# Kernel tuning notes

Measured on AMD Instinct MI355X. Metric: run time of the kernel, lower is better.

The kernel has to match this reference:

```python
import jax, jax.numpy as jnp
import numpy as np

D, NH, NL, NP, NLAYERS = 256, 8, 4, 4, 6
DH = D // NH
SHAPES = [(76, 100), (38, 50), (19, 25), (10, 13)]
STARTS = [int(s) for s in np.cumsum([0] + [h * w for h, w in SHAPES])[:-1]]
LQ = sum(h * w for h, w in SHAPES)
B = 2


def _layernorm(x, g, b, eps=1e-5):
    m = x.mean(-1, keepdims=True)
    v = ((x - m) ** 2).mean(-1, keepdims=True)
    return (x - m) * jax.lax.rsqrt(v + eps) * g + b


def _ref_points():
    pts = []
    for H, W in SHAPES:
        ry = (jnp.arange(H, dtype=jnp.float32) + 0.5) / H
        rx = (jnp.arange(W, dtype=jnp.float32) + 0.5) / W
        gy, gx = jnp.meshgrid(ry, rx, indexing='ij')
        pts.append(jnp.stack([gx.ravel(), gy.ravel()], -1))
    ref = jnp.concatenate(pts, 0)  # [LQ, 2] (x, y)
    return jnp.broadcast_to(ref[:, None, :], (LQ, NL, 2))


def _bilinear(v, loc, H, W):
    # v: [BN, H*W, DH]; loc: [BN, N, 2] normalized (x, y).
    # Matches torch grid_sample(align_corners=False, padding='zeros') with grid=2*loc-1.
    px = loc[..., 0] * W - 0.5
    py = loc[..., 1] * H - 0.5
    x0f = jnp.floor(px)
    y0f = jnp.floor(py)
    lx = px - x0f
    ly = py - y0f
    x0 = x0f.astype(jnp.int32)
    y0 = y0f.astype(jnp.int32)
    out = jnp.zeros(loc.shape[:-1] + (DH,), v.dtype)
    for dy, dx, w in ((0, 0, (1 - ly) * (1 - lx)), (0, 1, (1 - ly) * lx), (1, 0, ly * (1 - lx)), (1, 1, ly * lx)):
        xi = x0 + dx
        yi = y0 + dy
        valid = (xi >= 0) & (xi < W) & (yi >= 0) & (yi < H)
        idx = jnp.clip(yi, 0, H - 1) * W + jnp.clip(xi, 0, W - 1)
        g = jnp.take_along_axis(v, idx[..., None], axis=1)  # [BN, N, DH]
        out = out + g * (w * valid)[..., None]
    return out


def _layer(src, pos, ref, p):
    q = src + pos
    value = (src @ p['w_val'] + p['b_val']).reshape(B, LQ, NH, DH)
    off = (q @ p['w_off'] + p['b_off']).reshape(B, LQ, NH, NL, NP, 2)
    aw = jax.nn.softmax((q @ p['w_attn'] + p['b_attn']).reshape(B, LQ, NH, NL * NP), -1)
    aw = aw.reshape(B, LQ, NH, NL, NP)
    norm = jnp.array([[w, h] for h, w in SHAPES], jnp.float32)  # [NL, 2] = (W, H)
    loc = ref[None, :, None, :, None, :] + off / norm[None, None, None, :, None, :]  # [B,LQ,NH,NL,NP,2]
    v_t = value.transpose(0, 2, 1, 3).reshape(B * NH, LQ, DH)
    out = jnp.zeros((B, NH, LQ, DH), src.dtype)
    for l, (H, W) in enumerate(SHAPES):
        vl = v_t[:, STARTS[l]:STARTS[l] + H * W]
        locl = loc[:, :, :, l].transpose(0, 2, 1, 3, 4).reshape(B * NH, LQ * NP, 2)
        g = _bilinear(vl, locl, H, W).reshape(B, NH, LQ, NP, DH)
        out = out + jnp.einsum('bhqp,bhqpd->bhqd', aw[:, :, :, l].transpose(0, 2, 1, 3), g)
    attn = out.transpose(0, 2, 1, 3).reshape(B, LQ, D) @ p['w_out'] + p['b_out']
    src = _layernorm(src + attn, p['ln1_g'], p['ln1_b'])
    ffn = jax.nn.relu(src @ p['w_ffn1'] + p['b_ffn1']) @ p['w_ffn2'] + p['b_ffn2']
    return _layernorm(src + ffn, p['ln2_g'], p['ln2_b'])


def setup_inputs() -> dict:
    key = jax.random.key(0)
    ks = jax.random.split(key, 16)
    inp = {}
    for i, (H, W) in enumerate(SHAPES):
        inp[f'src{i}'] = jax.random.normal(ks[i], (B, D, H, W), jnp.float32)
        inp[f'pos{i}'] = jax.random.normal(ks[4 + i], (B, D, H, W), jnp.float32)
    inp['level_embed'] = jax.random.normal(ks[8], (NL, D), jnp.float32)
    s = 0.02
    inp['w_off'] = jax.random.normal(ks[9], (NLAYERS, D, NH * NL * NP * 2), jnp.float32) * s
    inp['b_off'] = jnp.zeros((NLAYERS, NH * NL * NP * 2), jnp.float32)
    inp['w_attn'] = jax.random.normal(ks[10], (NLAYERS, D, NH * NL * NP), jnp.float32) * s
    inp['b_attn'] = jnp.zeros((NLAYERS, NH * NL * NP), jnp.float32)
    inp['w_val'] = jax.random.normal(ks[11], (NLAYERS, D, D), jnp.float32) * s
    inp['b_val'] = jnp.zeros((NLAYERS, D), jnp.float32)
    inp['w_out'] = jax.random.normal(ks[12], (NLAYERS, D, D), jnp.float32) * s
    inp['b_out'] = jnp.zeros((NLAYERS, D), jnp.float32)
    inp['ln1_g'] = jnp.ones((NLAYERS, D), jnp.float32)
    inp['ln1_b'] = jnp.zeros((NLAYERS, D), jnp.float32)
    inp['w_ffn1'] = jax.random.normal(ks[13], (NLAYERS, D, 1024), jnp.float32) * s
    inp['b_ffn1'] = jnp.zeros((NLAYERS, 1024), jnp.float32)
    inp['w_ffn2'] = jax.random.normal(ks[14], (NLAYERS, 1024, D), jnp.float32) * s
    inp['b_ffn2'] = jnp.zeros((NLAYERS, D), jnp.float32)
    inp['ln2_g'] = jnp.ones((NLAYERS, D), jnp.float32)
    inp['ln2_b'] = jnp.zeros((NLAYERS, D), jnp.float32)
    return inp


def reference(src0, src1, src2, src3, pos0, pos1, pos2, pos3, level_embed,
              w_off, b_off, w_attn, b_attn, w_val, b_val, w_out, b_out,
              ln1_g, ln1_b, w_ffn1, b_ffn1, w_ffn2, b_ffn2, ln2_g, ln2_b):
    srcs = [src0, src1, src2, src3]
    poss = [pos0, pos1, pos2, pos3]
    src_flat = jnp.concatenate(
        [s.reshape(B, D, -1).transpose(0, 2, 1) + level_embed[l][None, None] for l, s in enumerate(srcs)], 1)
    pos_flat = jnp.concatenate([p.reshape(B, D, -1).transpose(0, 2, 1) for p in poss], 1)
    ref = _ref_points()
    x = src_flat
    for i in range(NLAYERS):
        p = dict(w_off=w_off[i], b_off=b_off[i], w_attn=w_attn[i], b_attn=b_attn[i],
                 w_val=w_val[i], b_val=b_val[i], w_out=w_out[i], b_out=b_out[i],
                 ln1_g=ln1_g[i], ln1_b=ln1_b[i], w_ffn1=w_ffn1[i], b_ffn1=b_ffn1[i],
                 w_ffn2=w_ffn2[i], b_ffn2=b_ffn2[i], ln2_g=ln2_g[i], ln2_b=ln2_b[i])
        x = _layer(x, pos_flat, ref, p)
    return x  # [B, LQ, D] encoded memory
```

## Files before the change

### kernel.cpp

```cpp
#include <hip/hip_runtime.h>
#include <math.h>

#define LQ 10105
#define BATCH 2
#define NLAYERS 6
#define NTOK (BATCH * LQ)

typedef __attribute__((ext_vector_type(8))) short bf16x8;
typedef __attribute__((ext_vector_type(4))) float f32x4;

__device__ inline unsigned short f2bf_rne(float f) {
    unsigned u = __float_as_uint(f);
    unsigned r = u + 0x7fffu + ((u >> 16) & 1u);
    return (unsigned short)(r >> 16);
}
__device__ inline float bf2f(unsigned short h) {
    return __uint_as_float((unsigned)h << 16);
}

__global__ __launch_bounds__(256)
void flatten_k(const float* __restrict__ src, const float* __restrict__ pos,
               const float* __restrict__ lvl, float* __restrict__ src_flat,
               float* __restrict__ pos_flat, int HW, int start)
{
    int hw = blockIdx.x;
    int b  = blockIdx.y;
    int d  = threadIdx.x;
    float sv = src[((size_t)b * 256 + d) * HW + hw];
    float pv = pos[((size_t)b * 256 + d) * HW + hw];
    size_t o = ((size_t)(b * LQ + start + hw)) * 256 + d;
    src_flat[o] = sv + lvl[d];
    pos_flat[o] = pv;
}

__global__ __launch_bounds__(256)
void wsplit_k(const float* __restrict__ W, unsigned short* __restrict__ Th,
              unsigned short* __restrict__ Tl, int K, int N,
              long srcStride, long dstStride)
{
    __shared__ float t[32][33];
    int layer = blockIdx.z;
    int n0 = blockIdx.x * 32, k0 = blockIdx.y * 32;
    int tx = threadIdx.x & 31, ty = threadIdx.x >> 5;
    const float* Wsrc = W + (size_t)layer * srcStride;
    #pragma unroll
    for (int i = 0; i < 4; ++i)
        t[ty + i * 8][tx] = Wsrc[(size_t)(k0 + ty + i * 8) * N + n0 + tx];
    __syncthreads();
    unsigned short* th = Th + (size_t)layer * dstStride;
    unsigned short* tl = Tl + (size_t)layer * dstStride;
    #pragma unroll
    for (int i = 0; i < 4; ++i) {
        int n = n0 + ty + i * 8;
        float v = t[tx][ty + i * 8];
        unsigned short h = f2bf_rne(v);
        th[(size_t)n * K + k0 + tx] = h;
        tl[(size_t)n * K + k0 + tx] = f2bf_rne(v - bf2f(h));
    }
}

__global__ void boa_k(const float* __restrict__ b_off,
                      const float* __restrict__ b_attn, float* __restrict__ boa)
{
    int l = blockIdx.x, t = threadIdx.x;
    boa[l * 384 + t] = (t < 256) ? b_off[l * 256 + t] : b_attn[l * 128 + (t - 256)];
}

template<bool HAS_A2, bool RELU, bool HAS_RES>
__global__ __launch_bounds__(256)
void gemm_mfma(const float* __restrict__ A, const float* __restrict__ A2,
               const unsigned short* __restrict__ Bh,
               const unsigned short* __restrict__ Bl,
               const float* __restrict__ bias, const float* __restrict__ Res,
               float* __restrict__ C, int M, int N, int K)
{
    __shared__ unsigned short sAh[128 * 32];
    __shared__ unsigned short sAl[128 * 32];
    __shared__ unsigned short sBh[128 * 32];
    __shared__ unsigned short sBl[128 * 32];

    const int tid = threadIdx.x;
    const int m0 = blockIdx.x * 128;
    const int n0 = blockIdx.y * 128;

    const int w  = tid >> 6;
    const int l  = tid & 63;
    const int wm = (w >> 1) * 64;
    const int wn = (w & 1) * 64;
    const int lr = l & 15;
    const int kb = (l >> 4) * 8;
    const int rr = (l >> 4) * 4;

    const int sm = tid >> 1;
    const int sk = (tid & 1) * 16;
    const int arow = m0 + sm;
    const bool aok = arow < M;

    f32x4 acc[4][4];
    #pragma unroll
    for (int i = 0; i < 4; ++i)
        #pragma unroll
        for (int j = 0; j < 4; ++j)
            acc[i][j] = (f32x4){0.f, 0.f, 0.f, 0.f};

    for (int kt = 0; kt < K; kt += 32) {
        float va[16];
        if (aok) {
            const float* ap = &A[(size_t)arow * K + kt + sk];
            *(float4*)&va[0]  = *(const float4*)(ap + 0);
            *(float4*)&va[4]  = *(const float4*)(ap + 4);
            *(float4*)&va[8]  = *(const float4*)(ap + 8);
            *(float4*)&va[12] = *(const float4*)(ap + 12);
            if (HAS_A2) {
                const float* ap2 = &A2[(size_t)arow * K + kt + sk];
                float4 t0 = *(const float4*)(ap2 + 0);
                float4 t1 = *(const float4*)(ap2 + 4);
                float4 t2 = *(const float4*)(ap2 + 8);
                float4 t3 = *(const float4*)(ap2 + 12);
                va[0] += t0.x; va[1] += t0.y; va[2]  += t0.z; va[3]  += t0.w;
                va[4] += t1.x; va[5] += t1.y; va[6]  += t1.z; va[7]  += t1.w;
                va[8] += t2.x; va[9] += t2.y; va[10] += t2.z; va[11] += t2.w;
                va[12]+= t3.x; va[13]+= t3.y; va[14] += t3.z; va[15] += t3.w;
            }
        } else {
            #pragma unroll
            for (int j = 0; j < 16; ++j) va[j] = 0.f;
        }
        const unsigned short* bph = &Bh[(size_t)(n0 + sm) * K + kt + sk];
        const unsigned short* bpl = &Bl[(size_t)(n0 + sm) * K + kt + sk];
        bf16x8 vbh0 = *(const bf16x8*)(bph);
        bf16x8 vbh1 = *(const bf16x8*)(bph + 8);
        bf16x8 vbl0 = *(const bf16x8*)(bpl);
        bf16x8 vbl1 = *(const bf16x8*)(bpl + 8);

        bf16x8 ah0, ah1, al0, al1;
        #pragma unroll
        for (int j = 0; j < 8; ++j) {
            float v0 = va[j], v1 = va[8 + j];
            unsigned short h0 = (unsigned short)(__float_as_uint(v0) >> 16);
            unsigned short h1 = (unsigned short)(__float_as_uint(v1) >> 16);
            ah0[j] = (short)h0;
            ah1[j] = (short)h1;
            float r0 = v0 - bf2f(h0);
            float r1 = v1 - bf2f(h1);
            al0[j] = (short)(unsigned short)(__float_as_uint(r0) >> 16);
            al1[j] = (short)(unsigned short)(__float_as_uint(r1) >> 16);
        }

        __syncthreads();
        *(bf16x8*)&sAh[sm * 32 + sk]     = ah0;
        *(bf16x8*)&sAh[sm * 32 + sk + 8] = ah1;
        *(bf16x8*)&sAl[sm * 32 + sk]     = al0;
        *(bf16x8*)&sAl[sm * 32 + sk + 8] = al1;
        *(bf16x8*)&sBh[sm * 32 + sk]     = vbh0;
        *(bf16x8*)&sBh[sm * 32 + sk + 8] = vbh1;
        *(bf16x8*)&sBl[sm * 32 + sk]     = vbl0;
        *(bf16x8*)&sBl[sm * 32 + sk + 8] = vbl1;
        __syncthreads();

        bf16x8 fah[4], fal[4];
        #pragma unroll
        for (int mf = 0; mf < 4; ++mf) {
            int off = (wm + mf * 16 + lr) * 32 + kb;
            fah[mf] = *(const bf16x8*)&sAh[off];
            fal[mf] = *(const bf16x8*)&sAl[off];
        }
        #pragma unroll
        for (int nf = 0; nf < 4; ++nf) {
            int boff = (wn + nf * 16 + lr) * 32 + kb;
            bf16x8 fbh = *(const bf16x8*)&sBh[boff];
            bf16x8 fbl = *(const bf16x8*)&sBl[boff];
            #pragma unroll
            for (int mf = 0; mf < 4; ++mf) {
                f32x4 c = acc[mf][nf];
                c = __builtin_amdgcn_mfma_f32_16x16x32_bf16(fah[mf], fbh, c, 0, 0, 0);
                c = __builtin_amdgcn_mfma_f32_16x16x32_bf16(fah[mf], fbl, c, 0, 0, 0);
                c = __builtin_amdgcn_mfma_f32_16x16x32_bf16(fal[mf], fbh, c, 0, 0, 0);
                acc[mf][nf] = c;
            }
        }
    }

    #pragma unroll
    for (int nf = 0; nf < 4; ++nf) {
        int col = n0 + wn + nf * 16 + lr;
        float bs = bias[col];
        #pragma unroll
        for (int mf = 0; mf < 4; ++mf) {
            int rowb = m0 + wm + mf * 16 + rr;
            #pragma unroll
            for (int r = 0; r < 4; ++r) {
                int row = rowb + r;
                if (row < M) {
                    float v = acc[mf][nf][r] + bs;
                    if (HAS_RES) v += Res[(size_t)row * N + col];
                    if (RELU) v = fmaxf(v, 0.f);
                    C[(size_t)row * N + col] = v;
                }
            }
        }
    }
}

__global__ __launch_bounds__(256)
void sample_k(const float* __restrict__ val, const float* __restrict__ oab,
              float* __restrict__ out)
{
    const int Hs[4] = {76, 38, 19, 10};
    const int Ws[4] = {100, 50, 25, 13};
    const int ST[4] = {0, 7600, 9500, 9975};

    int bid = blockIdx.x;
    int xcd = bid & 7;
    const int qch = LQ >> 3;
    const int rem = LQ & 7;
    int q = (xcd < rem ? xcd * (qch + 1) : rem * (qch + 1) + (xcd - rem) * qch)
            + (bid >> 3);
    int b = blockIdx.y;
    int tid = threadIdx.x;

    __shared__ int2 s_iw[512];

    if (tid < 128) {
        int h = tid >> 4, pt = tid & 15, lvl = pt >> 2, p = pt & 3;
        int lq, local;
        if (q < 7600)      { lq = 0; local = q; }
        else if (q < 9500) { lq = 1; local = q - 7600; }
        else if (q < 9975) { lq = 2; local = q - 9500; }
        else               { lq = 3; local = q - 9975; }
        int Wq = Ws[lq], Hq = Hs[lq];
        int ry = local / Wq, rx = local - ry * Wq;
        float refx = (rx + 0.5f) / (float)Wq;
        float refy = (ry + 0.5f) / (float)Hq;

        size_t rowb = (size_t)(b * LQ + q) * 384;
        float logit = oab[rowb + 256 + h * 16 + pt];
        float mx = logit;
        mx = fmaxf(mx, __shfl_xor(mx, 1, 64));
        mx = fmaxf(mx, __shfl_xor(mx, 2, 64));
        mx = fmaxf(mx, __shfl_xor(mx, 4, 64));
        mx = fmaxf(mx, __shfl_xor(mx, 8, 64));
        float e = expf(logit - mx);
        float s = e;
        s += __shfl_xor(s, 1, 64);
        s += __shfl_xor(s, 2, 64);
        s += __shfl_xor(s, 4, 64);
        s += __shfl_xor(s, 8, 64);
        float aw = e / s;

        float ox = oab[rowb + h * 32 + lvl * 8 + p * 2];
        float oy = oab[rowb + h * 32 + lvl * 8 + p * 2 + 1];
        int W = Ws[lvl], H = Hs[lvl], st = ST[lvl];
        float px = refx * (float)W + ox - 0.5f;
        float py = refy * (float)H + oy - 0.5f;
        float x0f = floorf(px), y0f = floorf(py);
        float lx = px - x0f, ly = py - y0f;
        int x0 = (int)x0f, y0 = (int)y0f;
        int x1 = x0 + 1, y1 = y0 + 1;
        float ax0 = ((x0 >= 0) & (x0 < W)) ? (1.f - lx) : 0.f;
        float ax1 = ((x1 >= 0) & (x1 < W)) ? lx : 0.f;
        float ay0 = ((y0 >= 0) & (y0 < H)) ? (1.f - ly) : 0.f;
        float ay1 = ((y1 >= 0) & (y1 < H)) ? ly : 0.f;
        int cx0 = min(max(x0, 0), W - 1), cx1 = min(max(x1, 0), W - 1);
        int cy0 = min(max(y0, 0), H - 1), cy1 = min(max(y1, 0), H - 1);
        int i00 = st + cy0 * W + cx0, i01 = st + cy0 * W + cx1;
        int i10 = st + cy1 * W + cx0, i11 = st + cy1 * W + cx1;
        int base4 = tid * 4;
        s_iw[base4 + 0] = make_int2(i00, __float_as_int(aw * ay0 * ax0));
        s_iw[base4 + 1] = make_int2(i01, __float_as_int(aw * ay0 * ax1));
        s_iw[base4 + 2] = make_int2(i10, __float_as_int(aw * ay1 * ax0));
        s_iw[base4 + 3] = make_int2(i11, __float_as_int(aw * ay1 * ax1));
    }
    __syncthreads();

    int lane   = tid & 63;
    int wv     = tid >> 6;
    int h      = wv * 2 + (lane >> 5);
    int half   = lane & 31;
    int corner = half >> 3;
    int c4     = half & 7;
    const float* vb = val + (size_t)(b * LQ) * 256 + h * 32 + c4 * 4;
    int sbase = h * 64 + corner;

    float4 acc = make_float4(0.f, 0.f, 0.f, 0.f);
    #pragma unroll
    for (int pt = 0; pt < 16; ++pt) {
        int2 iw = s_iw[sbase + pt * 4];
        float wgt = __int_as_float(iw.y);
        float4 v = *(const float4*)&vb[(size_t)iw.x * 256];
        acc.x += wgt * v.x; acc.y += wgt * v.y;
        acc.z += wgt * v.z; acc.w += wgt * v.w;
    }
    acc.x += __shfl_xor(acc.x, 8, 64);  acc.y += __shfl_xor(acc.y, 8, 64);
    acc.z += __shfl_xor(acc.z, 8, 64);  acc.w += __shfl_xor(acc.w, 8, 64);
    acc.x += __shfl_xor(acc.x, 16, 64); acc.y += __shfl_xor(acc.y, 16, 64);
    acc.z += __shfl_xor(acc.z, 16, 64); acc.w += __shfl_xor(acc.w, 16, 64);

    if (corner == 0)
        *(float4*)&out[(size_t)(b * LQ + q) * 256 + h * 32 + c4 * 4] = acc;
}

__global__ __launch_bounds__(256)
void ln_k(const float* __restrict__ x, const float* __restrict__ g,
          const float* __restrict__ bt, float* __restrict__ out, int nrows)
{
    int row = blockIdx.x * 4 + (threadIdx.x >> 6);
    int lane = threadIdx.x & 63;
    if (row >= nrows) return;

    float4 v = *(const float4*)&x[(size_t)row * 256 + lane * 4];
    float s = v.x + v.y + v.z + v.w;
    #pragma unroll
    for (int o = 32; o > 0; o >>= 1) s += __shfl_down(s, o, 64);
    s = __shfl(s, 0, 64);
    float m = s * (1.0f / 256.0f);
    float cx = v.x - m, cy = v.y - m, cz = v.z - m, cw = v.w - m;
    float s2 = cx * cx + cy * cy + cz * cz + cw * cw;
    #pragma unroll
    for (int o = 32; o > 0; o >>= 1) s2 += __shfl_down(s2, o, 64);
    s2 = __shfl(s2, 0, 64);
    float rstd = rsqrtf(s2 * (1.0f / 256.0f) + 1e-5f);

    float4 gv = *(const float4*)&g[lane * 4];
    float4 bv = *(const float4*)&bt[lane * 4];
    float4 r;
    r.x = cx * rstd * gv.x + bv.x;
    r.y = cy * rstd * gv.y + bv.y;
    r.z = cz * rstd * gv.z + bv.z;
    r.w = cw * rstd * gv.w + bv.w;
    *(float4*)&out[(size_t)row * 256 + lane * 4] = r;
}

extern "C" void kernel_launch(void* const* d_in, const int* in_sizes, int n_in,
                              void* d_out, int out_size, void* d_ws, size_t ws_size,
                              hipStream_t stream)
{
    const float* src_in[4] = {(const float*)d_in[0], (const float*)d_in[2],
                              (const float*)d_in[4], (const float*)d_in[6]};
    const float* pos_in[4] = {(const float*)d_in[1], (const float*)d_in[3],
                              (const float*)d_in[5], (const float*)d_in[7]};
    const float* lvl    = (const float*)d_in[8];
    const float* w_off  = (const float*)d_in[9];
    const float* b_off  = (const float*)d_in[10];
    const float* w_attn = (const float*)d_in[11];
    const float* b_attn = (const float*)d_in[12];
    const float* w_val  = (const float*)d_in[13];
    const float* b_val  = (const float*)d_in[14];
    const float* w_out  = (const float*)d_in[15];
    const float* b_out  = (const float*)d_in[16];
    const float* ln1_g  = (const float*)d_in[17];
    const float* ln1_b  = (const float*)d_in[18];
    const float* w_ffn1 = (const float*)d_in[19];
    const float* b_ffn1 = (const float*)d_in[20];
    const float* w_ffn2 = (const float*)d_in[21];
    const float* b_ffn2 = (const float*)d_in[22];
    const float* ln2_g  = (const float*)d_in[23];
    const float* ln2_b  = (const float*)d_in[24];

    float* ws    = (float*)d_ws;
    float* src   = ws;
    float* pos   = src   + (size_t)NTOK * 256;
    float* preln = pos   + (size_t)NTOK * 256;
    float* uni   = preln + (size_t)NTOK * 256;
    float* valb  = uni;
    float* oab   = uni + (size_t)NTOK * 256;
    float* samp  = oab + (size_t)NTOK * 384;
    float* ffnb  = uni;
    float* boa   = uni + (size_t)NTOK * 1024;
    unsigned short* Wh = (unsigned short*)(boa + 6 * 384);
    const long WL = 753664;
    unsigned short* Wl = Wh + (size_t)NLAYERS * WL;
    const long O_VAL = 0, O_OFF = 65536, O_ATT = 131072, O_OUT = 163840,
               O_F1 = 229376, O_F2 = 491520;

    wsplit_k<<<dim3(8, 8, 6),  256, 0, stream>>>(w_val,  Wh + O_VAL, Wl + O_VAL, 256, 256,  65536, WL);
    wsplit_k<<<dim3(8, 8, 6),  256, 0, stream>>>(w_off,  Wh + O_OFF, Wl + O_OFF, 256, 256,  65536, WL);
    wsplit_k<<<dim3(4, 8, 6),  256, 0, stream>>>(w_attn, Wh + O_ATT, Wl + O_ATT, 256, 128,  32768, WL);
    wsplit_k<<<dim3(8, 8, 6),  256, 0, stream>>>(w_out,  Wh + O_OUT, Wl + O_OUT, 256, 256,  65536, WL);
    wsplit_k<<<dim3(32, 8, 6), 256, 0, stream>>>(w_ffn1, Wh + O_F1,  Wl + O_F1,  256, 1024, 262144, WL);
    wsplit_k<<<dim3(8, 32, 6), 256, 0, stream>>>(w_ffn2, Wh + O_F2,  Wl + O_F2,  1024, 256, 262144, WL);
    boa_k<<<dim3(6), dim3(384), 0, stream>>>(b_off, b_attn, boa);

    const int HWs[4] = {7600, 1900, 475, 130};
    const int STt[4] = {0, 7600, 9500, 9975};
    for (int l = 0; l < 4; ++l) {
        dim3 g(HWs[l], BATCH);
        flatten_k<<<g, 256, 0, stream>>>(src_in[l], pos_in[l], lvl + l * 256,
                                         src, pos, HWs[l], STt[l]);
    }

    const int MB = (NTOK + 127) / 128;
    const int LNB = (NTOK + 3) / 4;
    dim3 blk(256);

    for (int i = 0; i < NLAYERS; ++i) {
        const unsigned short* whL = Wh + (size_t)i * WL;
        const unsigned short* wlL = Wl + (size_t)i * WL;
        const float* bv  = b_val  + (size_t)i * 256;
        const float* bou = b_out  + (size_t)i * 256;
        const float* l1g = ln1_g  + (size_t)i * 256;
        const float* l1b = ln1_b  + (size_t)i * 256;
        const float* bf1 = b_ffn1 + (size_t)i * 1024;
        const float* bf2 = b_ffn2 + (size_t)i * 256;
        const float* l2g = ln2_g  + (size_t)i * 256;
        const float* l2b = ln2_b  + (size_t)i * 256;

        gemm_mfma<false, false, false><<<dim3(MB, 2), blk, 0, stream>>>(
            src, nullptr, whL + O_VAL, wlL + O_VAL, bv, nullptr, valb, NTOK, 256, 256);
        gemm_mfma<true, false, false><<<dim3(MB, 3), blk, 0, stream>>>(
            src, pos, whL + O_OFF, wlL + O_OFF, boa + (size_t)i * 384, nullptr,
            oab, NTOK, 384, 256);
        sample_k<<<dim3(LQ, BATCH), blk, 0, stream>>>(valb, oab, samp);
        gemm_mfma<false, false, true><<<dim3(MB, 2), blk, 0, stream>>>(
            samp, nullptr, whL + O_OUT, wlL + O_OUT, bou, src, preln, NTOK, 256, 256);
        ln_k<<<dim3(LNB), blk, 0, stream>>>(preln, l1g, l1b, src, NTOK);
        gemm_mfma<false, true, false><<<dim3(MB, 8), blk, 0, stream>>>(
            src, nullptr, whL + O_F1, wlL + O_F1, bf1, nullptr, ffnb, NTOK, 1024, 256);
        gemm_mfma<false, false, true><<<dim3(MB, 2), blk, 0, stream>>>(
            ffnb, nullptr, whL + O_F2, wlL + O_F2, bf2, src, preln, NTOK, 256, 1024);
        float* dst = (i == NLAYERS - 1) ? (float*)d_out : src;
        ln_k<<<dim3(LNB), blk, 0, stream>>>(preln, l2g, l2b, dst, NTOK);
    }
}
```

Baseline: 1.922 ms.

## Store value/sample/FFN intermediates in bf16, add XCD tile remap and LDS padding

The value projection, sampled features and FFN hidden activations are now written in bf16 instead of fp32. The consuming GEMMs read bf16 A directly, dropping the A low-part plane and one of three MFMAs per fragment. The GEMM also moves to a 1D grid with an XCD-aware block-to-tile remap, and pads LDS rows to 40 to reduce bank conflicts. This cuts memory traffic and MFMA work on the large intermediates, at the cost of bf16 rounding error in activations that were previously kept near fp32 precision.

Result: faster. 1.756 ms (-8.6%).

```diff
diff --git a/kernel.cpp b/kernel.cpp
--- a/kernel.cpp
+++ b/kernel.cpp
@@ -66,23 +66,32 @@
     boa[l * 384 + t] = (t < 256) ? b_off[l * 256 + t] : b_attn[l * 128 + (t - 256)];
 }
 
-template<bool HAS_A2, bool RELU, bool HAS_RES>
+template<bool A_BF16, bool HAS_A2, bool RELU, bool HAS_RES, bool C_BF16>
 __global__ __launch_bounds__(256)
-void gemm_mfma(const float* __restrict__ A, const float* __restrict__ A2,
+void gemm_mfma(const void* __restrict__ Av, const float* __restrict__ A2,
                const unsigned short* __restrict__ Bh,
                const unsigned short* __restrict__ Bl,
                const float* __restrict__ bias, const float* __restrict__ Res,
-               float* __restrict__ C, int M, int N, int K)
-{
-    __shared__ unsigned short sAh[128 * 32];
-    __shared__ unsigned short sAl[128 * 32];
-    __shared__ unsigned short sBh[128 * 32];
-    __shared__ unsigned short sBl[128 * 32];
+               void* __restrict__ Cv, int M, int N, int K, int NB)
+{
+    constexpr int LDR = 40;
+    constexpr int PLANES = A_BF16 ? 3 : 4;
+    __shared__ unsigned short sMem[PLANES * 128 * LDR];
+    unsigned short* sBh = sMem;
+    unsigned short* sBl = sMem + 128 * LDR;
+    unsigned short* sAh = sMem + 2 * 128 * LDR;
+    unsigned short* sAl = sMem + (PLANES - 1) * 128 * LDR;
+
+    const int nwg = gridDim.x;
+    const int bid = blockIdx.x;
+    const int q8 = nwg >> 3, r8 = nwg & 7, xcd = bid & 7;
+    const int work = (xcd < r8 ? xcd * (q8 + 1) : r8 * (q8 + 1) + (xcd - r8) * q8)
+                     + (bid >> 3);
+    const int mblk = work / NB;
+    const int m0 = mblk * 128;
+    const int n0 = (work - mblk * NB) * 128;
 
     const int tid = threadIdx.x;
-    const int m0 = blockIdx.x * 128;
-    const int n0 = blockIdx.y * 128;
-
     const int w  = tid >> 6;
     const int l  = tid & 63;
     const int wm = (w >> 1) * 64;
@@ -104,28 +113,6 @@
             acc[i][j] = (f32x4){0.f, 0.f, 0.f, 0.f};
 
     for (int kt = 0; kt < K; kt += 32) {
-        float va[16];
-        if (aok) {
-            const float* ap = &A[(size_t)arow * K + kt + sk];
-            *(float4*)&va[0]  = *(const float4*)(ap + 0);
-            *(float4*)&va[4]  = *(const float4*)(ap + 4);
-            *(float4*)&va[8]  = *(const float4*)(ap + 8);
-            *(float4*)&va[12] = *(const float4*)(ap + 12);
-            if (HAS_A2) {
-                const float* ap2 = &A2[(size_t)arow * K + kt + sk];
-                float4 t0 = *(const float4*)(ap2 + 0);
-                float4 t1 = *(const float4*)(ap2 + 4);
-                float4 t2 = *(const float4*)(ap2 + 8);
-                float4 t3 = *(const float4*)(ap2 + 12);
-                va[0] += t0.x; va[1] += t0.y; va[2]  += t0.z; va[3]  += t0.w;
-                va[4] += t1.x; va[5] += t1.y; va[6]  += t1.z; va[7]  += t1.w;
-                va[8] += t2.x; va[9] += t2.y; va[10] += t2.z; va[11] += t2.w;
-                va[12]+= t3.x; va[13]+= t3.y; va[14] += t3.z; va[15] += t3.w;
-            }
-        } else {
-            #pragma unroll
-            for (int j = 0; j < 16; ++j) va[j] = 0.f;
-        }
         const unsigned short* bph = &Bh[(size_t)(n0 + sm) * K + kt + sk];
         const unsigned short* bpl = &Bl[(size_t)(n0 + sm) * K + kt + sk];
         bf16x8 vbh0 = *(const bf16x8*)(bph);
@@ -133,41 +120,74 @@
         bf16x8 vbl0 = *(const bf16x8*)(bpl);
         bf16x8 vbl1 = *(const bf16x8*)(bpl + 8);
 
-        bf16x8 ah0, ah1, al0, al1;
-        #pragma unroll
-        for (int j = 0; j < 8; ++j) {
-            float v0 = va[j], v1 = va[8 + j];
-            unsigned short h0 = (unsigned short)(__float_as_uint(v0) >> 16);
-            unsigned short h1 = (unsigned short)(__float_as_uint(v1) >> 16);
-            ah0[j] = (short)h0;
-            ah1[j] = (short)h1;
-            float r0 = v0 - bf2f(h0);
-            float r1 = v1 - bf2f(h1);
-            al0[j] = (short)(unsigned short)(__float_as_uint(r0) >> 16);
-            al1[j] = (short)(unsigned short)(__float_as_uint(r1) >> 16);
+        bf16x8 ah0 = {}, ah1 = {}, al0 = {}, al1 = {};
+        if constexpr (A_BF16) {
+            if (aok) {
+                const unsigned short* ap =
+                    (const unsigned short*)Av + (size_t)arow * K + kt + sk;
+                ah0 = *(const bf16x8*)ap;
+                ah1 = *(const bf16x8*)(ap + 8);
+            }
+        } else {
+            float va[16];
+            if (aok) {
+                const float* ap = (const float*)Av + (size_t)arow * K + kt + sk;
+                *(float4*)&va[0]  = *(const float4*)(ap + 0);
+                *(float4*)&va[4]  = *(const float4*)(ap + 4);
+                *(float4*)&va[8]  = *(const float4*)(ap + 8);
+                *(float4*)&va[12] = *(const float4*)(ap + 12);
+                if (HAS_A2) {
+                    const float* ap2 = &A2[(size_t)arow * K + kt + sk];
+                    float4 t0 = *(const float4*)(ap2 + 0);
+                    float4 t1 = *(const float4*)(ap2 + 4);
+                    float4 t2 = *(const float4*)(ap2 + 8);
+                    float4 t3 = *(const float4*)(ap2 + 12);
+                    va[0] += t0.x; va[1] += t0.y; va[2]  += t0.z; va[3]  += t0.w;
+                    va[4] += t1.x; va[5] += t1.y; va[6]  += t1.z; va[7]  += t1.w;
+                    va[8] += t2.x; va[9] += t2.y; va[10] += t2.z; va[11] += t2.w;
+                    va[12]+= t3.x; va[13]+= t3.y; va[14] += t3.z; va[15] += t3.w;
+                }
+            } else {
+                #pragma unroll
+                for (int j = 0; j < 16; ++j) va[j] = 0.f;
+            }
+            #pragma unroll
+            for (int j = 0; j < 8; ++j) {
+                float v0 = va[j], v1 = va[8 + j];
+                unsigned short h0 = (unsigned short)(__float_as_uint(v0) >> 16);
+                unsigned short h1 = (unsigned short)(__float_as_uint(v1) >> 16);
+                ah0[j] = (short)h0;
+                ah1[j] = (short)h1;
+                float r0 = v0 - bf2f(h0);
+                float r1 = v1 - bf2f(h1);
+                al0[j] = (short)(unsigned short)(__float_as_uint(r0) >> 16);
+                al1[j] = (short)(unsigned short)(__float_as_uint(r1) >> 16);
+            }
         }
 
         __syncthreads();
-        *(bf16x8*)&sAh[sm * 32 + sk]     = ah0;
-        *(bf16x8*)&sAh[sm * 32 + sk + 8] = ah1;
-        *(bf16x8*)&sAl[sm * 32 + sk]     = al0;
-        *(bf16x8*)&sAl[sm * 32 + sk + 8] = al1;
-        *(bf16x8*)&sBh[sm * 32 + sk]     = vbh0;
-        *(bf16x8*)&sBh[sm * 32 + sk + 8] = vbh1;
-        *(bf16x8*)&sBl[sm * 32 + sk]     = vbl0;
-        *(bf16x8*)&sBl[sm * 32 + sk + 8] = vbl1;
+        *(bf16x8*)&sAh[sm * LDR + sk]     = ah0;
+        *(bf16x8*)&sAh[sm * LDR + sk + 8] = ah1;
+        if constexpr (!A_BF16) {
+            *(bf16x8*)&sAl[sm * LDR + sk]     = al0;
+            *(bf16x8*)&sAl[sm * LDR + sk + 8] = al1;
+        }
+        *(bf16x8*)&sBh[sm * LDR + sk]     = vbh0;
+        *(bf16x8*)&sBh[sm * LDR + sk + 8] = vbh1;
+        *(bf16x8*)&sBl[sm * LDR + sk]     = vbl0;
+        *(bf16x8*)&sBl[sm * LDR + sk + 8] = vbl1;
         __syncthreads();
 
         bf16x8 fah[4], fal[4];
         #pragma unroll
         for (int mf = 0; mf < 4; ++mf) {
-            int off = (wm + mf * 16 + lr) * 32 + kb;
+            int off = (wm + mf * 16 + lr) * LDR + kb;
             fah[mf] = *(const bf16x8*)&sAh[off];
-            fal[mf] = *(const bf16x8*)&sAl[off];
+            if constexpr (!A_BF16) fal[mf] = *(const bf16x8*)&sAl[off];
         }
         #pragma unroll
         for (int nf = 0; nf < 4; ++nf) {
-            int boff = (wn + nf * 16 + lr) * 32 + kb;
+            int boff = (wn + nf * 16 + lr) * LDR + kb;
             bf16x8 fbh = *(const bf16x8*)&sBh[boff];
             bf16x8 fbl = *(const bf16x8*)&sBl[boff];
             #pragma unroll
@@ -175,12 +195,15 @@
                 f32x4 c = acc[mf][nf];
                 c = __builtin_amdgcn_mfma_f32_16x16x32_bf16(fah[mf], fbh, c, 0, 0, 0);
                 c = __builtin_amdgcn_mfma_f32_16x16x32_bf16(fah[mf], fbl, c, 0, 0, 0);
-                c = __builtin_amdgcn_mfma_f32_16x16x32_bf16(fal[mf], fbh, c, 0, 0, 0);
+                if constexpr (!A_BF16)
+                    c = __builtin_amdgcn_mfma_f32_16x16x32_bf16(fal[mf], fbh, c, 0, 0, 0);
                 acc[mf][nf] = c;
             }
         }
     }
 
+    float* Cf = (float*)Cv;
+    unsigned short* Cb = (unsigned short*)Cv;
     #pragma unroll
     for (int nf = 0; nf < 4; ++nf) {
         int col = n0 + wn + nf * 16 + lr;
@@ -195,7 +218,10 @@
                     float v = acc[mf][nf][r] + bs;
                     if (HAS_RES) v += Res[(size_t)row * N + col];
                     if (RELU) v = fmaxf(v, 0.f);
-                    C[(size_t)row * N + col] = v;
+                    if constexpr (C_BF16)
+                        Cb[(size_t)row * N + col] = f2bf_rne(v);
+                    else
+                        Cf[(size_t)row * N + col] = v;
                 }
             }
         }
@@ -203,8 +229,8 @@
 }
 
 __global__ __launch_bounds__(256)
-void sample_k(const float* __restrict__ val, const float* __restrict__ oab,
-              float* __restrict__ out)
+void sample_k(const unsigned short* __restrict__ val,
+              const float* __restrict__ oab, unsigned short* __restrict__ out)
 {
     const int Hs[4] = {76, 38, 19, 10};
     const int Ws[4] = {100, 50, 25, 13};
@@ -279,7 +305,7 @@
     int half   = lane & 31;
     int corner = half >> 3;
     int c4     = half & 7;
-    const float* vb = val + (size_t)(b * LQ) * 256 + h * 32 + c4 * 4;
+    const unsigned short* vb = val + (size_t)(b * LQ) * 256 + h * 32 + c4 * 4;
     int sbase = h * 64 + corner;
 
     float4 acc = make_float4(0.f, 0.f, 0.f, 0.f);
@@ -287,17 +313,21 @@
     for (int pt = 0; pt < 16; ++pt) {
         int2 iw = s_iw[sbase + pt * 4];
         float wgt = __int_as_float(iw.y);
-        float4 v = *(const float4*)&vb[(size_t)iw.x * 256];
-        acc.x += wgt * v.x; acc.y += wgt * v.y;
-        acc.z += wgt * v.z; acc.w += wgt * v.w;
+        ushort4 v = *(const ushort4*)&vb[(size_t)iw.x * 256];
+        acc.x += wgt * bf2f(v.x); acc.y += wgt * bf2f(v.y);
+        acc.z += wgt * bf2f(v.z); acc.w += wgt * bf2f(v.w);
     }
     acc.x += __shfl_xor(acc.x, 8, 64);  acc.y += __shfl_xor(acc.y, 8, 64);
     acc.z += __shfl_xor(acc.z, 8, 64);  acc.w += __shfl_xor(acc.w, 8, 64);
     acc.x += __shfl_xor(acc.x, 16, 64); acc.y += __shfl_xor(acc.y, 16, 64);
     acc.z += __shfl_xor(acc.z, 16, 64); acc.w += __shfl_xor(acc.w, 16, 64);
 
-    if (corner == 0)
-        *(float4*)&out[(size_t)(b * LQ + q) * 256 + h * 32 + c4 * 4] = acc;
+    if (corner == 0) {
+        ushort4 o;
+        o.x = f2bf_rne(acc.x); o.y = f2bf_rne(acc.y);
+        o.z = f2bf_rne(acc.z); o.w = f2bf_rne(acc.w);
+        *(ushort4*)&out[(size_t)(b * LQ + q) * 256 + h * 32 + c4 * 4] = o;
+    }
 }
 
 __global__ __launch_bounds__(256)
@@ -361,12 +391,12 @@
     float* src   = ws;
     float* pos   = src   + (size_t)NTOK * 256;
     float* preln = pos   + (size_t)NTOK * 256;
-    float* uni   = preln + (size_t)NTOK * 256;
-    float* valb  = uni;
-    float* oab   = uni + (size_t)NTOK * 256;
-    float* samp  = oab + (size_t)NTOK * 384;
-    float* ffnb  = uni;
-    float* boa   = uni + (size_t)NTOK * 1024;
+    char*  uni   = (char*)(preln + (size_t)NTOK * 256);
+    unsigned short* valb = (unsigned short*)uni;
+    float* oab = (float*)(uni + (size_t)NTOK * 512);
+    unsigned short* samp = (unsigned short*)(uni + (size_t)NTOK * 2048);
+    unsigned short* ffnb = (unsigned short*)uni;
+    float* boa = (float*)(uni + (size_t)NTOK * 2560);
     unsigned short* Wh = (unsigned short*)(boa + 6 * 384);
     const long WL = 753664;
     unsigned short* Wl = Wh + (size_t)NLAYERS * WL;
@@ -405,19 +435,19 @@
         const float* l2g = ln2_g  + (size_t)i * 256;
         const float* l2b = ln2_b  + (size_t)i * 256;
 
-        gemm_mfma<false, false, false><<<dim3(MB, 2), blk, 0, stream>>>(
-            src, nullptr, whL + O_VAL, wlL + O_VAL, bv, nullptr, valb, NTOK, 256, 256);
-        gemm_mfma<true, false, false><<<dim3(MB, 3), blk, 0, stream>>>(
+        gemm_mfma<false, false, false, false, true><<<dim3(MB * 2), blk, 0, stream>>>(
+            src, nullptr, whL + O_VAL, wlL + O_VAL, bv, nullptr, valb, NTOK, 256, 256, 2);
+        gemm_mfma<false, true, false, false, false><<<dim3(MB * 3), blk, 0, stream>>>(
             src, pos, whL + O_OFF, wlL + O_OFF, boa + (size_t)i * 384, nullptr,
-            oab, NTOK, 384, 256);
+            oab, NTOK, 384, 256, 3);
         sample_k<<<dim3(LQ, BATCH), blk, 0, stream>>>(valb, oab, samp);
-        gemm_mfma<false, false, true><<<dim3(MB, 2), blk, 0, stream>>>(
-            samp, nullptr, whL + O_OUT, wlL + O_OUT, bou, src, preln, NTOK, 256, 256);
+        gemm_mfma<true, false, false, true, false><<<dim3(MB * 2), blk, 0, stream>>>(
+            samp, nullptr, whL + O_OUT, wlL + O_OUT, bou, src, preln, NTOK, 256, 256, 2);
         ln_k<<<dim3(LNB), blk, 0, stream>>>(preln, l1g, l1b, src, NTOK);
-        gemm_mfma<false, true, false><<<dim3(MB, 8), blk, 0, stream>>>(
-            src, nullptr, whL + O_F1, wlL + O_F1, bf1, nullptr, ffnb, NTOK, 1024, 256);
-        gemm_mfma<false, false, true><<<dim3(MB, 2), blk, 0, stream>>>(
-            ffnb, nullptr, whL + O_F2, wlL + O_F2, bf2, src, preln, NTOK, 256, 1024);
+        gemm_mfma<false, false, true, false, true><<<dim3(MB * 8), blk, 0, stream>>>(
+            src, nullptr, whL + O_F1, wlL + O_F1, bf1, nullptr, ffnb, NTOK, 1024, 256, 8);
+        gemm_mfma<true, false, false, true, false><<<dim3(MB * 2), blk, 0, stream>>>(
+            ffnb, nullptr, whL + O_F2, wlL + O_F2, bf2, src, preln, NTOK, 256, 1024, 2);
         float* dst = (i == NLAYERS - 1) ? (float*)d_out : src;
         ln_k<<<dim3(LNB), blk, 0, stream>>>(preln, l2g, l2b, dst, NTOK);
     }
```
